# Kernel tuning notes

Hardware: AMD Instinct MI355X
Metric: run time of the kernel (lower is better)

## Reference

```python
import jax, jax.numpy as jnp
import numpy as np

B, S, T, D = 4, 512, 512, 256


def setup_inputs() -> dict:
    key = jax.random.key(0)
    ks = jax.random.split(key, 10)
    scale = 1.0 / np.sqrt(D)
    return {
        "source": jax.random.normal(ks[0], (B, S, D), jnp.float32),
        "target": jax.random.normal(ks[1], (B, T, D), jnp.float32),
        "W_src": jax.random.uniform(ks[2], (D, D), jnp.float32, -scale, scale),
        "b_src": jax.random.uniform(ks[3], (D,), jnp.float32, -scale, scale),
        "W_tgt": jax.random.uniform(ks[4], (D, D), jnp.float32, -scale, scale),
        "b_tgt": jax.random.uniform(ks[5], (D,), jnp.float32, -scale, scale),
        "W_res": jax.random.uniform(ks[6], (D, 1), jnp.float32, -scale, scale),
        "b_res": jax.random.uniform(ks[7], (1,), jnp.float32, -scale, scale),
        "W_prob": jax.random.uniform(ks[8], (D, 2), jnp.float32, -scale, scale),
        "b_prob": jax.random.uniform(ks[9], (2,), jnp.float32, -scale, scale),
    }


def reference(source, target, W_src, b_src, W_tgt, b_tgt, W_res, b_res, W_prob, b_prob):
    # source: (B,S,D), target: (B,T,D)
    src_lin = jnp.einsum("bsd,de->bse", source, W_src) + b_src  # (B,S,D)
    tgt_lin = jnp.einsum("btd,de->bte", target, W_tgt) + b_tgt  # (B,T,D)
    # Bahdanau-style additive attention: (B,T,S,D) broadcast, tanh, D->1
    h = jnp.tanh(src_lin[:, None, :, :] + tgt_lin[:, :, None, :])  # (B,T,S,D)
    genP = jnp.einsum("btsd,d->bts", h, W_res[:, 0]) + b_res[0]     # (B,T,S)
    prob = jax.nn.softmax(jnp.einsum("btd,de->bte", target, W_prob) + b_prob, axis=-1)  # (B,T,2)
    return genP, prob
```

## Files before the change

kernel.cpp:

```cpp
#include <hip/hip_runtime.h>

#define B_ 4
#define S_ 512
#define T_ 512
#define D_ 256
#define NSRC (B_ * S_)
#define NROW 4096
#define K2F 2.8853900817779268f

typedef __attribute__((ext_vector_type(8))) short short8;
typedef __attribute__((ext_vector_type(8))) _Float16 half8;
typedef __attribute__((ext_vector_type(4))) float f32x4;
typedef __attribute__((ext_vector_type(2))) float f32x2;

__device__ __forceinline__ unsigned short f2bf(float f) {
    union { float f; unsigned u; } v; v.f = f;
    unsigned r = v.u + 0x7FFF + ((v.u >> 16) & 1);
    return (unsigned short)(r >> 16);
}

__global__ __launch_bounds__(256) void ysyt_kernel(
    const float* __restrict__ src, const float* __restrict__ tgt,
    const float* __restrict__ Wsrc, const float* __restrict__ Wtgt,
    const float* __restrict__ Wp,  const float* __restrict__ bp,
    const float* __restrict__ bsrc, const float* __restrict__ btgt,
    _Float16* __restrict__ ytr, float* __restrict__ out)
{
    __shared__ unsigned short lwt[16384];
    __shared__ _Float16 ltb[64][72];
    const int bid = blockIdx.x, tid = threadIdx.x;
    const int lane = tid & 63, w = tid >> 6;

    if (bid < 256) {
        const int rowblk = bid >> 2, colq = bid & 3;
        const int R0 = rowblk * 64;
        const int n = lane & 15, quad = lane >> 4;
        const int mat = (R0 >= NSRC) ? 1 : 0;
        const float* bias = mat ? btgt : bsrc;
        const float* Wm = mat ? Wtgt : Wsrc;
        const float* xb = mat ? &tgt[(R0 - NSRC) * D_] : &src[R0 * D_];

        {
            const int r = tid;
            const int ksr = r >> 5, qr = (r >> 3) & 3, jr = r & 7;
            const int wbase = ksr * 512 + qr * 8 + jr;
            #pragma unroll 4
            for (int i = 0; i < 16; i++) {
                float4 v = *(const float4*)&Wm[r * D_ + colq * 64 + 4 * i];
                const int cc = 4 * i;
                lwt[((cc + 0) >> 4) * 4096 + ((cc + 0) & 15) * 32 + wbase] = f2bf(v.x);
                lwt[((cc + 1) >> 4) * 4096 + ((cc + 1) & 15) * 32 + wbase] = f2bf(v.y);
                lwt[((cc + 2) >> 4) * 4096 + ((cc + 2) & 15) * 32 + wbase] = f2bf(v.z);
                lwt[((cc + 3) >> 4) * 4096 + ((cc + 3) & 15) * 32 + wbase] = f2bf(v.w);
            }
        }

        short8 af[8];
        #pragma unroll
        for (int ks = 0; ks < 8; ks++) {
            const float* p = &xb[(w * 16 + n) * D_ + ks * 32 + quad * 8];
            float4 u0 = *(const float4*)p;
            float4 u1 = *(const float4*)(p + 4);
            short8 v;
            v[0] = (short)f2bf(u0.x); v[1] = (short)f2bf(u0.y);
            v[2] = (short)f2bf(u0.z); v[3] = (short)f2bf(u0.w);
            v[4] = (short)f2bf(u1.x); v[5] = (short)f2bf(u1.y);
            v[6] = (short)f2bf(u1.z); v[7] = (short)f2bf(u1.w);
            af[ks] = v;
        }
        __syncthreads();

        #pragma unroll
        for (int gc = 0; gc < 4; gc++) {
            const int gcol = colq * 4 + gc;
            const unsigned short* bp2 = &lwt[gc * 4096 + n * 32 + quad * 8];
            short8 bf[8];
            #pragma unroll
            for (int ks = 0; ks < 8; ks++) bf[ks] = *(const short8*)&bp2[ks * 512];
            f32x4 a4 = {0.f, 0.f, 0.f, 0.f};
            #pragma unroll
            for (int ks = 0; ks < 8; ks++)
                a4 = __builtin_amdgcn_mfma_f32_16x16x32_bf16(af[ks], bf[ks], a4, 0, 0, 0);
            const float bv = bias[gcol * 16 + n];
            const int rl = w * 16 + quad * 4;
            const int dl = gc * 16 + n;
            ltb[rl + 0][dl] = (_Float16)fminf(__builtin_amdgcn_exp2f((a4[0] + bv) * K2F), 60000.f);
            ltb[rl + 1][dl] = (_Float16)fminf(__builtin_amdgcn_exp2f((a4[1] + bv) * K2F), 60000.f);
            ltb[rl + 2][dl] = (_Float16)fminf(__builtin_amdgcn_exp2f((a4[2] + bv) * K2F), 60000.f);
            ltb[rl + 3][dl] = (_Float16)fminf(__builtin_amdgcn_exp2f((a4[3] + bv) * K2F), 60000.f);
        }
        __syncthreads();
        {
            const int row = tid >> 2, seg = tid & 3;
            half8 v0 = *(const half8*)&ltb[row][seg * 16];
            half8 v1 = *(const half8*)&ltb[row][seg * 16 + 8];
            _Float16* dst = &ytr[(size_t)(R0 + row) * D_ + colq * 64 + seg * 16];
            *(half8*)&dst[0] = v0;
            *(half8*)&dst[8] = v1;
        }
    } else {
        int row  = (bid - 256) * 4 + w;
        float p0 = 0.f, p1 = 0.f;
        #pragma unroll
        for (int i = 0; i < 4; i++) {
            int d = lane + i * 64;
            float v = tgt[row * D_ + d];
            float2 wv = *(const float2*)&Wp[d * 2];
            p0 = fmaf(v, wv.x, p0);
            p1 = fmaf(v, wv.y, p1);
        }
        #pragma unroll
        for (int off = 32; off > 0; off >>= 1) {
            p0 += __shfl_down(p0, off, 64);
            p1 += __shfl_down(p1, off, 64);
        }
        if (lane == 0) {
            const float L2E = 1.4426950408889634f;
            float l0 = p0 + bp[0], l1 = p1 + bp[1];
            float e10 = __builtin_amdgcn_exp2f((l1 - l0) * L2E);
            float e01 = __builtin_amdgcn_exp2f((l0 - l1) * L2E);
            out[B_ * T_ * S_ + row * 2 + 0] = __builtin_amdgcn_rcpf(1.f + e10);
            out[B_ * T_ * S_ + row * 2 + 1] = __builtin_amdgcn_rcpf(1.f + e01);
        }
    }
}

__global__ __launch_bounds__(256) void genp_kernel(
    const _Float16* __restrict__ ytr,
    const float* __restrict__ Wres, const float* __restrict__ bres,
    float* __restrict__ out)
{
    __shared__ _Float16 lys[2][32][72];
    __shared__ _Float16 lyt[2][32][72];

    const int tid = threadIdx.x;
    const int lane = tid & 63;
    const int s0 = blockIdx.x * 32;
    const int t0 = blockIdx.y * 32;
    const int b  = blockIdx.z;
    const int m  = tid & 15;
    const int g  = tid >> 4;

    const int srow = tid & 31;
    const int sq   = (tid >> 5) & 7;
    const size_t gsbase = (size_t)(b * S_ + s0 + srow) * D_;
    const size_t gtbase = (size_t)(NSRC + b * T_ + t0 + srow) * D_;

    half8 pvs = *(const half8*)&ytr[gsbase + 8 * sq];
    half8 pvt = *(const half8*)&ytr[gtbase + 8 * sq];
    *(half8*)&lys[0][srow][8 * sq] = pvs;
    *(half8*)&lyt[0][srow][8 * sq] = pvt;
    __syncthreads();

    f32x2 acc[2];
    acc[0] = (f32x2){0.f, 0.f};
    acc[1] = (f32x2){0.f, 0.f};
    const f32x2 one2 = {1.f, 1.f};

    for (int c = 0; c < 4; c++) {
        const int bi = c & 1;
        half8 nvs, nvt;
        if (c < 3) {
            nvs = *(const half8*)&ytr[gsbase + (c + 1) * 64 + 8 * sq];
            nvt = *(const half8*)&ytr[gtbase + (c + 1) * 64 + 8 * sq];
        }
        const float* wp = &Wres[c * 64];
        #pragma unroll 2
        for (int kq = 0; kq < 8; kq++) {
            half8 sL = *(const half8*)&lys[bi][m][8 * kq];
            half8 sH = *(const half8*)&lys[bi][m + 16][8 * kq];
            half8 tL = *(const half8*)&lyt[bi][g][8 * kq];
            half8 tH = *(const half8*)&lyt[bi][g + 16][8 * kq];
            f32x2 sp[8];
            float tLf[8], tHf[8];
            f32x2 wv[8];
            #pragma unroll
            for (int k = 0; k < 8; k++) {
                sp[k] = (f32x2){(float)sL[k], (float)sH[k]};
                tLf[k] = (float)tL[k];
                tHf[k] = (float)tH[k];
                const float wk = wp[kq * 8 + k];
                wv[k] = (f32x2){wk, wk};
            }
            #define FOLD(TT, TF) {                                            \
                f32x2 dd[8];                                                  \
                _Pragma("unroll")                                             \
                for (int k = 0; k < 8; k++) {                                 \
                    const f32x2 cs2 = {TF[k], TF[k]};                         \
                    dd[k] = sp[k] * cs2 + one2;                               \
                }                                                             \
                f32x2 p01 = dd[0] * dd[1];                                    \
                f32x2 p23 = dd[2] * dd[3];                                    \
                f32x2 p45 = dd[4] * dd[5];                                    \
                f32x2 p67 = dd[6] * dd[7];                                    \
                f32x2 q03 = p01 * p23;                                        \
                f32x2 q47 = p45 * p67;                                        \
                f32x2 den = q03 * q47;                                        \
                f32x2 u01 = dd[1] * wv[0]; u01 = dd[0] * wv[1] + u01;         \
                f32x2 u23 = dd[3] * wv[2]; u23 = dd[2] * wv[3] + u23;         \
                f32x2 u45 = dd[5] * wv[4]; u45 = dd[4] * wv[5] + u45;         \
                f32x2 u67 = dd[7] * wv[6]; u67 = dd[6] * wv[7] + u67;         \
                f32x2 n03 = u01 * p23; n03 = u23 * p01 + n03;                 \
                f32x2 n47 = u45 * p67; n47 = u67 * p45 + n47;                 \
                f32x2 num = n03 * q47; num = n47 * q03 + num;                 \
                f32x2 rr;                                                     \
                rr.x = __builtin_amdgcn_rcpf(den.x);                          \
                rr.y = __builtin_amdgcn_rcpf(den.y);                          \
                acc[TT] = num * rr + acc[TT];                                 \
            }
            FOLD(0, tLf) FOLD(1, tHf)
            #undef FOLD
        }
        if (c < 3) {
            *(half8*)&lys[bi ^ 1][srow][8 * sq] = nvs;
            *(half8*)&lyt[bi ^ 1][srow][8 * sq] = nvt;
        }
        __syncthreads();
    }

    float cw = Wres[lane] + Wres[lane + 64] + Wres[lane + 128] + Wres[lane + 192];
    #pragma unroll
    for (int off = 32; off > 0; off >>= 1) cw += __shfl_xor(cw, off, 64);
    const float C0 = cw + bres[0];

    out[(size_t)(b * T_ + t0 + g     ) * S_ + s0 + m     ] = C0 - 2.f * acc[0].x;
    out[(size_t)(b * T_ + t0 + g     ) * S_ + s0 + m + 16] = C0 - 2.f * acc[0].y;
    out[(size_t)(b * T_ + t0 + g + 16) * S_ + s0 + m     ] = C0 - 2.f * acc[1].x;
    out[(size_t)(b * T_ + t0 + g + 16) * S_ + s0 + m + 16] = C0 - 2.f * acc[1].y;
}

extern "C" void kernel_launch(void* const* d_in, const int* in_sizes, int n_in,
                              void* d_out, int out_size, void* d_ws, size_t ws_size,
                              hipStream_t stream) {
    const float* source = (const float*)d_in[0];
    const float* target = (const float*)d_in[1];
    const float* W_src  = (const float*)d_in[2];
    const float* b_src  = (const float*)d_in[3];
    const float* W_tgt  = (const float*)d_in[4];
    const float* b_tgt  = (const float*)d_in[5];
    const float* W_res  = (const float*)d_in[6];
    const float* b_res  = (const float*)d_in[7];
    const float* W_prob = (const float*)d_in[8];
    const float* b_prob = (const float*)d_in[9];
    float* out = (float*)d_out;

    _Float16* ytr = (_Float16*)d_ws;

    ysyt_kernel<<<768, 256, 0, stream>>>(source, target, W_src, W_tgt,
                                         W_prob, b_prob, b_src, b_tgt,
                                         ytr, out);
    genp_kernel<<<dim3(16, 16, 4), 256, 0, stream>>>(ytr, W_res, b_res, out);
}
```

Baseline: 108.4 us.

## Load full D-slab into LDS once instead of double-buffered 64-wide chunks

The genp kernel now stages the whole 32x256 source and target fp16 tiles into shared memory up front. It then runs a single 32-iteration loop with no per-chunk barriers or register prefetch. This removes three __syncthreads and the prefetch bookkeeping. In exchange, LDS use per block grows from about 18KB to about 33KB, which may reduce occupancy, and the global load latency is no longer overlapped with compute.

```diff
diff --git a/kernel.cpp b/kernel.cpp
--- a/kernel.cpp
+++ b/kernel.cpp
@@ -130,8 +130,8 @@
     const float* __restrict__ Wres, const float* __restrict__ bres,
     float* __restrict__ out)
 {
-    __shared__ _Float16 lys[2][32][72];
-    __shared__ _Float16 lyt[2][32][72];
+    __shared__ _Float16 lys[32][264];
+    __shared__ _Float16 lyt[32][264];
 
     const int tid = threadIdx.x;
     const int lane = tid & 63;
@@ -141,15 +141,17 @@
     const int m  = tid & 15;
     const int g  = tid >> 4;
 
-    const int srow = tid & 31;
-    const int sq   = (tid >> 5) & 7;
-    const size_t gsbase = (size_t)(b * S_ + s0 + srow) * D_;
-    const size_t gtbase = (size_t)(NSRC + b * T_ + t0 + srow) * D_;
-
-    half8 pvs = *(const half8*)&ytr[gsbase + 8 * sq];
-    half8 pvt = *(const half8*)&ytr[gtbase + 8 * sq];
-    *(half8*)&lys[0][srow][8 * sq] = pvs;
-    *(half8*)&lyt[0][srow][8 * sq] = pvt;
+    {
+        const int srow = tid >> 3;
+        const int seg  = tid & 7;
+        const size_t gs = (size_t)(b * S_ + s0 + srow) * D_ + seg * 32;
+        const size_t gt = (size_t)(NSRC + b * T_ + t0 + srow) * D_ + seg * 32;
+        #pragma unroll
+        for (int j = 0; j < 4; j++) {
+            *(half8*)&lys[srow][seg * 32 + 8 * j] = *(const half8*)&ytr[gs + 8 * j];
+            *(half8*)&lyt[srow][seg * 32 + 8 * j] = *(const half8*)&ytr[gt + 8 * j];
+        }
+    }
     __syncthreads();
 
     f32x2 acc[2];
@@ -157,65 +159,51 @@
     acc[1] = (f32x2){0.f, 0.f};
     const f32x2 one2 = {1.f, 1.f};
 
-    for (int c = 0; c < 4; c++) {
-        const int bi = c & 1;
-        half8 nvs, nvt;
-        if (c < 3) {
-            nvs = *(const half8*)&ytr[gsbase + (c + 1) * 64 + 8 * sq];
-            nvt = *(const half8*)&ytr[gtbase + (c + 1) * 64 + 8 * sq];
-        }
-        const float* wp = &Wres[c * 64];
-        #pragma unroll 2
-        for (int kq = 0; kq < 8; kq++) {
-            half8 sL = *(const half8*)&lys[bi][m][8 * kq];
-            half8 sH = *(const half8*)&lys[bi][m + 16][8 * kq];
-            half8 tL = *(const half8*)&lyt[bi][g][8 * kq];
-            half8 tH = *(const half8*)&lyt[bi][g + 16][8 * kq];
-            f32x2 sp[8];
-            float tLf[8], tHf[8];
-            f32x2 wv[8];
-            #pragma unroll
-            for (int k = 0; k < 8; k++) {
-                sp[k] = (f32x2){(float)sL[k], (float)sH[k]};
-                tLf[k] = (float)tL[k];
-                tHf[k] = (float)tH[k];
-                const float wk = wp[kq * 8 + k];
-                wv[k] = (f32x2){wk, wk};
-            }
-            #define FOLD(TT, TF) {                                            \
-                f32x2 dd[8];                                                  \
-                _Pragma("unroll")                                             \
-                for (int k = 0; k < 8; k++) {                                 \
-                    const f32x2 cs2 = {TF[k], TF[k]};                         \
-                    dd[k] = sp[k] * cs2 + one2;                               \
-                }                                                             \
-                f32x2 p01 = dd[0] * dd[1];                                    \
-                f32x2 p23 = dd[2] * dd[3];                                    \
-                f32x2 p45 = dd[4] * dd[5];                                    \
-                f32x2 p67 = dd[6] * dd[7];                                    \
-                f32x2 q03 = p01 * p23;                                        \
-                f32x2 q47 = p45 * p67;                                        \
-                f32x2 den = q03 * q47;                                        \
-                f32x2 u01 = dd[1] * wv[0]; u01 = dd[0] * wv[1] + u01;         \
-                f32x2 u23 = dd[3] * wv[2]; u23 = dd[2] * wv[3] + u23;         \
-                f32x2 u45 = dd[5] * wv[4]; u45 = dd[4] * wv[5] + u45;         \
-                f32x2 u67 = dd[7] * wv[6]; u67 = dd[6] * wv[7] + u67;         \
-                f32x2 n03 = u01 * p23; n03 = u23 * p01 + n03;                 \
-                f32x2 n47 = u45 * p67; n47 = u67 * p45 + n47;                 \
-                f32x2 num = n03 * q47; num = n47 * q03 + num;                 \
-                f32x2 rr;                                                     \
-                rr.x = __builtin_amdgcn_rcpf(den.x);                          \
-                rr.y = __builtin_amdgcn_rcpf(den.y);                          \
-                acc[TT] = num * rr + acc[TT];                                 \
-            }
-            FOLD(0, tLf) FOLD(1, tHf)
-            #undef FOLD
-        }
-        if (c < 3) {
-            *(half8*)&lys[bi ^ 1][srow][8 * sq] = nvs;
-            *(half8*)&lyt[bi ^ 1][srow][8 * sq] = nvt;
-        }
-        __syncthreads();
+    #pragma unroll 4
+    for (int kq = 0; kq < 32; kq++) {
+        half8 sL = *(const half8*)&lys[m][8 * kq];
+        half8 sH = *(const half8*)&lys[m + 16][8 * kq];
+        half8 tL = *(const half8*)&lyt[g][8 * kq];
+        half8 tH = *(const half8*)&lyt[g + 16][8 * kq];
+        f32x2 sp[8];
+        float tLf[8], tHf[8];
+        f32x2 wv[8];
+        #pragma unroll
+        for (int k = 0; k < 8; k++) {
+            sp[k] = (f32x2){(float)sL[k], (float)sH[k]};
+            tLf[k] = (float)tL[k];
+            tHf[k] = (float)tH[k];
+            const float wk = Wres[kq * 8 + k];
+            wv[k] = (f32x2){wk, wk};
+        }
+        #define FOLD(TT, TF) {                                            \
+            f32x2 dd[8];                                                  \
+            _Pragma("unroll")                                             \
+            for (int k = 0; k < 8; k++) {                                 \
+                const f32x2 cs2 = {TF[k], TF[k]};                         \
+                dd[k] = sp[k] * cs2 + one2;                               \
+            }                                                             \
+            f32x2 p01 = dd[0] * dd[1];                                    \
+            f32x2 p23 = dd[2] * dd[3];                                    \
+            f32x2 p45 = dd[4] * dd[5];                                    \
+            f32x2 p67 = dd[6] * dd[7];                                    \
+            f32x2 q03 = p01 * p23;                                        \
+            f32x2 q47 = p45 * p67;                                        \
+            f32x2 den = q03 * q47;                                        \
+            f32x2 u01 = dd[1] * wv[0]; u01 = dd[0] * wv[1] + u01;         \
+            f32x2 u23 = dd[3] * wv[2]; u23 = dd[2] * wv[3] + u23;         \
+            f32x2 u45 = dd[5] * wv[4]; u45 = dd[4] * wv[5] + u45;         \
+            f32x2 u67 = dd[7] * wv[6]; u67 = dd[6] * wv[7] + u67;         \
+            f32x2 n03 = u01 * p23; n03 = u23 * p01 + n03;                 \
+            f32x2 n47 = u45 * p67; n47 = u67 * p45 + n47;                 \
+            f32x2 num = n03 * q47; num = n47 * q03 + num;                 \
+            f32x2 rr;                                                     \
+            rr.x = __builtin_amdgcn_rcpf(den.x);                          \
+            rr.y = __builtin_amdgcn_rcpf(den.y);                          \
+            acc[TT] = num * rr + acc[TT];                                 \
+        }
+        FOLD(0, tLf) FOLD(1, tHf)
+        #undef FOLD
     }
 
     float cw = Wres[lane] + Wres[lane + 64] + Wres[lane + 128] + Wres[lane + 192];
```

After: 107.6 us. No clear change (-0.8%).
